# Performance work log

Measured on AMD Instinct MI355X. Metric: run time of the kernel, lower is better.

Reference implementation:

```python
import jax, jax.numpy as jnp
import numpy as np

N_NODES = 100000
N_EDGES = 1600000
IN_DIM, HIDDEN, OUT = 256, 128, 64


def setup_inputs() -> dict:
    key = jax.random.key(0)
    k1, k2, k3, k4 = jax.random.split(key, 4)
    x = jax.random.normal(k1, (N_NODES, IN_DIM), dtype=jnp.float32)
    edge_index = jax.random.randint(k2, (2, N_EDGES), 0, N_NODES, dtype=jnp.int32)
    # glorot-ish init for the GCN linear layers
    W1 = jax.random.normal(k3, (IN_DIM, HIDDEN), dtype=jnp.float32) / np.sqrt(IN_DIM)
    b1 = jnp.zeros((HIDDEN,), dtype=jnp.float32)
    W2 = jax.random.normal(k4, (HIDDEN, OUT), dtype=jnp.float32) / np.sqrt(HIDDEN)
    b2 = jnp.zeros((OUT,), dtype=jnp.float32)
    return {"x": x, "edge_index": edge_index, "W1": W1, "b1": b1, "W2": W2, "b2": b2}


def gcn_layer(x, src, dst, W, b):
    """PyG GCNConv: add self-loops, symmetric deg^-1/2 normalization,
    linear transform, scatter-add aggregation, bias."""
    h = x @ W  # [N, F_out]
    # degree over self-looped graph: in-degree(dst counts) + 1 self loop
    deg = jax.ops.segment_sum(jnp.ones((src.shape[0],), h.dtype), dst,
                              num_segments=N_NODES) + 1.0
    dinv = jax.lax.rsqrt(deg)  # [N]
    coef = dinv[src] * dinv[dst]  # [E]
    agg = jax.ops.segment_sum(h[src] * coef[:, None], dst, num_segments=N_NODES)
    # self-loop contribution (norm = dinv[i]^2) without materializing loop edges
    agg = agg + h * (dinv * dinv)[:, None]
    return agg + b


def reference(x, edge_index, W1, b1, W2, b2):
    src, dst = edge_index[0], edge_index[1]
    h = jax.nn.relu(gcn_layer(x, src, dst, W1, b1))
    return jax.nn.relu(gcn_layer(h, src, dst, W2, b2))
```

## Files before the change

kernel.cpp:

```cpp
#include <hip/hip_runtime.h>

#define N_NODES 100000
#define N_EDGES 1600000
#define IN_DIM 256
#define HIDDEN 128
#define OUT_DIM 64

#define NBIN 391
#define NBLK3 256
#define CHUNK 6250
#define NMAT (NBIN * NBLK3)
#define NBLK_SCAN (NMAT / 256)
#define CAP 6144

typedef __bf16 bf16x8 __attribute__((ext_vector_type(8)));
typedef __bf16 bf16x4 __attribute__((ext_vector_type(4)));
typedef float f32x4 __attribute__((ext_vector_type(4)));

__launch_bounds__(256)
__global__ void k_hist(const int* __restrict__ dst, int* __restrict__ cnt2) {
    __shared__ int hist[NBIN];
    for (int i = threadIdx.x; i < NBIN; i += 256) hist[i] = 0;
    __syncthreads();
    int base = blockIdx.x * CHUNK;
    for (int i = threadIdx.x; i < CHUNK; i += 256)
        atomicAdd(&hist[dst[base + i] >> 8], 1);
    __syncthreads();
    for (int k = threadIdx.x; k < NBIN; k += 256)
        cnt2[k * NBLK3 + blockIdx.x] = hist[k];
}

__global__ void k_scan1(int* __restrict__ a, int* __restrict__ bsum) {
    __shared__ int tmp[256];
    int t = threadIdx.x;
    int i = blockIdx.x * 256 + t;
    int v = a[i];
    tmp[t] = v;
    __syncthreads();
    #pragma unroll
    for (int off = 1; off < 256; off <<= 1) {
        int p = (t >= off) ? tmp[t - off] : 0;
        __syncthreads();
        tmp[t] += p;
        __syncthreads();
    }
    a[i] = tmp[t] - v;
    if (t == 255) bsum[blockIdx.x] = tmp[255];
}

__global__ void k_scan2(int* __restrict__ bsum) {
    __shared__ int tmp[512];
    int t = threadIdx.x;
    int v = (t < NBLK_SCAN) ? bsum[t] : 0;
    tmp[t] = v;
    __syncthreads();
    #pragma unroll
    for (int off = 1; off < 512; off <<= 1) {
        int p = (t >= off) ? tmp[t - off] : 0;
        __syncthreads();
        tmp[t] += p;
        __syncthreads();
    }
    if (t < NBLK_SCAN) bsum[t] = tmp[t] - v;
}

__launch_bounds__(256)
__global__ void k_scatter_bins(const int* __restrict__ src, const int* __restrict__ dst,
                               const int* __restrict__ off2, const int* __restrict__ bsum,
                               unsigned int* __restrict__ ebuf) {
    __shared__ int cursor[NBIN];
    for (int k = threadIdx.x; k < NBIN; k += 256)
        cursor[k] = off2[k * NBLK3 + blockIdx.x] + bsum[k];
    __syncthreads();
    int base = blockIdx.x * CHUNK;
    for (int i = threadIdx.x; i < CHUNK; i += 256) {
        int s = src[base + i], d = dst[base + i];
        int pos = atomicAdd(&cursor[d >> 8], 1);
        ebuf[pos] = ((unsigned)s << 8) | (unsigned)(d & 255);
    }
}

__launch_bounds__(256)
__global__ void k_fine(const unsigned int* __restrict__ ebuf, const int* __restrict__ off2,
                       const int* __restrict__ bsum,
                       int* __restrict__ esrc, int* __restrict__ rowstart,
                       float* __restrict__ dinv) {
    __shared__ int hist[256];
    __shared__ int tmp[256];
    __shared__ int nodeoff[256];
    __shared__ int cursor[256];
    __shared__ unsigned int ed[CAP];
    __shared__ int sOut[CAP];

    const int k = blockIdx.x;
    const int t = threadIdx.x;
    const int e0 = off2[k * NBLK3] + bsum[k];
    const int e1 = (k + 1 < NBIN) ? off2[(k + 1) * NBLK3] + bsum[k + 1] : N_EDGES;
    int m = e1 - e0;
    if (m > CAP) m = CAP;

    hist[t] = 0;
    __syncthreads();
    for (int i = t; i < m; i += 256) {
        unsigned v = ebuf[e0 + i];
        ed[i] = v;
        atomicAdd(&hist[v & 255], 1);
    }
    __syncthreads();

    int v = hist[t];
    tmp[t] = v;
    __syncthreads();
    #pragma unroll
    for (int off = 1; off < 256; off <<= 1) {
        int p = (t >= off) ? tmp[t - off] : 0;
        __syncthreads();
        tmp[t] += p;
        __syncthreads();
    }
    nodeoff[t] = tmp[t] - v;
    cursor[t] = tmp[t] - v;
    __syncthreads();

    for (int i = t; i < m; i += 256) {
        unsigned e = ed[i];
        int pos = atomicAdd(&cursor[e & 255], 1);
        sOut[pos] = (int)(e >> 8);
    }
    __syncthreads();

    for (int i = t; i < m; i += 256) esrc[e0 + i] = sOut[i];

    int n = k * 256 + t;
    if (n < N_NODES) {
        rowstart[n] = e0 + nodeoff[t];
        dinv[n] = rsqrtf((float)hist[t] + 1.0f);
    }
    if (k == 0 && t == 0) rowstart[N_NODES] = N_EDGES;
}

__device__ __forceinline__ int bsw1h(int c, int kk) {
    return c * 128 + (kk ^ ((c & 7) << 3));
}

__launch_bounds__(512, 4)
__global__ void k_gemm1(const float* __restrict__ X, const float* __restrict__ W1,
                        __bf16* __restrict__ H) {
    __shared__ __attribute__((aligned(16))) __bf16 Bs[128 * 128];

    const int t = threadIdx.x;
    const int wave = t >> 6;
    const int lane = t & 63;
    const int lm = lane & 15;
    const int q = lane >> 4;
    const int row0 = blockIdx.x * 128;
    const int g = row0 + wave * 16 + lm;

    f32x4 acc[8] = {};

    for (int half = 0; half < 2; ++half) {
        __syncthreads();
        for (int p = 0; p < 4; ++p) {
            int i = t + 512 * p;
            int c = i & 127;
            int kg = i >> 7;
            float v[8];
            #pragma unroll
            for (int j = 0; j < 8; ++j)
                v[j] = W1[(half * 128 + kg * 8 + j) * HIDDEN + c];
            bf16x8 w;
            #pragma unroll
            for (int j = 0; j < 8; ++j) w[j] = (__bf16)v[j];
            *(bf16x8*)&Bs[bsw1h(c, kg * 8)] = w;
        }
        __syncthreads();

        #pragma unroll
        for (int k0 = 0; k0 < 128; k0 += 32) {
            float4 v0 = make_float4(0.f, 0.f, 0.f, 0.f), v1 = v0;
            if (g < N_NODES) {
                const float* p = &X[(size_t)g * IN_DIM + half * 128 + k0 + q * 8];
                v0 = *(const float4*)p;
                v1 = *(const float4*)(p + 4);
            }
            bf16x8 a;
            a[0] = (__bf16)v0.x; a[1] = (__bf16)v0.y;
            a[2] = (__bf16)v0.z; a[3] = (__bf16)v0.w;
            a[4] = (__bf16)v1.x; a[5] = (__bf16)v1.y;
            a[6] = (__bf16)v1.z; a[7] = (__bf16)v1.w;
            #pragma unroll
            for (int ni = 0; ni < 8; ++ni) {
                bf16x8 bfr = *(const bf16x8*)&Bs[bsw1h(ni * 16 + lm, k0 + q * 8)];
                acc[ni] = __builtin_amdgcn_mfma_f32_16x16x32_bf16(a, bfr, acc[ni], 0, 0, 0);
            }
        }
    }

    #pragma unroll
    for (int r = 0; r < 4; ++r) {
        int grow = row0 + wave * 16 + q * 4 + r;
        if (grow < N_NODES) {
            #pragma unroll
            for (int ni = 0; ni < 8; ++ni)
                H[grow * HIDDEN + ni * 16 + lm] = (__bf16)acc[ni][r];
        }
    }
}

__launch_bounds__(256)
__global__ void k_gather1(const int* __restrict__ rowstart, const int* __restrict__ esrc,
                          const float* __restrict__ dinv,
                          const __bf16* __restrict__ H, const float* __restrict__ b1,
                          __bf16* __restrict__ AGG) {
    int n = blockIdx.x * 16 + (threadIdx.x >> 4);
    if (n >= N_NODES) return;
    int j = (threadIdx.x & 15) * 8;

    float dn = dinv[n];
    float s = dn * dn;
    bf16x8 h = *(const bf16x8*)&H[n * HIDDEN + j];
    float acc[8];
    #pragma unroll
    for (int i = 0; i < 8; ++i) acc[i] = (float)h[i] * s;

    int p0 = rowstart[n], p1 = rowstart[n + 1];
    int p = p0;
    for (; p + 3 < p1; p += 4) {
        int s0 = esrc[p + 0], s1 = esrc[p + 1], s2 = esrc[p + 2], s3 = esrc[p + 3];
        float c0 = dinv[s0] * dn, c1 = dinv[s1] * dn;
        float c2 = dinv[s2] * dn, c3 = dinv[s3] * dn;
        bf16x8 v0 = *(const bf16x8*)&H[s0 * HIDDEN + j];
        bf16x8 v1 = *(const bf16x8*)&H[s1 * HIDDEN + j];
        bf16x8 v2 = *(const bf16x8*)&H[s2 * HIDDEN + j];
        bf16x8 v3 = *(const bf16x8*)&H[s3 * HIDDEN + j];
        #pragma unroll
        for (int i = 0; i < 8; ++i) acc[i] = fmaf((float)v0[i], c0, acc[i]);
        #pragma unroll
        for (int i = 0; i < 8; ++i) acc[i] = fmaf((float)v1[i], c1, acc[i]);
        #pragma unroll
        for (int i = 0; i < 8; ++i) acc[i] = fmaf((float)v2[i], c2, acc[i]);
        #pragma unroll
        for (int i = 0; i < 8; ++i) acc[i] = fmaf((float)v3[i], c3, acc[i]);
    }
    for (; p < p1; ++p) {
        int sidx = esrc[p];
        float c = dinv[sidx] * dn;
        bf16x8 v = *(const bf16x8*)&H[sidx * HIDDEN + j];
        #pragma unroll
        for (int i = 0; i < 8; ++i) acc[i] = fmaf((float)v[i], c, acc[i]);
    }

    float4 bb0 = *(const float4*)&b1[j];
    float4 bb1 = *(const float4*)&b1[j + 4];
    bf16x8 o;
    o[0] = (__bf16)fmaxf(acc[0] + bb0.x, 0.f);
    o[1] = (__bf16)fmaxf(acc[1] + bb0.y, 0.f);
    o[2] = (__bf16)fmaxf(acc[2] + bb0.z, 0.f);
    o[3] = (__bf16)fmaxf(acc[3] + bb0.w, 0.f);
    o[4] = (__bf16)fmaxf(acc[4] + bb1.x, 0.f);
    o[5] = (__bf16)fmaxf(acc[5] + bb1.y, 0.f);
    o[6] = (__bf16)fmaxf(acc[6] + bb1.z, 0.f);
    o[7] = (__bf16)fmaxf(acc[7] + bb1.w, 0.f);
    *(bf16x8*)&AGG[n * HIDDEN + j] = o;
}

__device__ __forceinline__ int bsw2(int c, int kk) {
    return c * 128 + (kk ^ ((c & 7) << 3));
}

__launch_bounds__(512, 8)
__global__ void k_gemm2(const __bf16* __restrict__ AGG, const float* __restrict__ W2,
                        __bf16* __restrict__ H2) {
    __shared__ __attribute__((aligned(16))) __bf16 Bs[64 * 128];

    const int t = threadIdx.x;
    const int wave = t >> 6;
    const int lane = t & 63;
    const int lm = lane & 15;
    const int q = lane >> 4;
    const int row0 = blockIdx.x * 128;
    const int g = row0 + wave * 16 + lm;

    for (int p = 0; p < 2; ++p) {
        int i = t + 512 * p;
        int c = i & 63;
        int kg = i >> 6;
        float v[8];
        #pragma unroll
        for (int j = 0; j < 8; ++j)
            v[j] = W2[(kg * 8 + j) * OUT_DIM + c];
        bf16x8 w;
        #pragma unroll
        for (int j = 0; j < 8; ++j) w[j] = (__bf16)v[j];
        *(bf16x8*)&Bs[bsw2(c, kg * 8)] = w;
    }
    __syncthreads();

    f32x4 acc[4] = {};

    #pragma unroll
    for (int k0 = 0; k0 < HIDDEN; k0 += 32) {
        bf16x8 a = {};
        if (g < N_NODES)
            a = *(const bf16x8*)&AGG[(size_t)g * HIDDEN + k0 + q * 8];
        #pragma unroll
        for (int ni = 0; ni < 4; ++ni) {
            bf16x8 bfr = *(const bf16x8*)&Bs[bsw2(ni * 16 + lm, k0 + q * 8)];
            acc[ni] = __builtin_amdgcn_mfma_f32_16x16x32_bf16(a, bfr, acc[ni], 0, 0, 0);
        }
    }

    #pragma unroll
    for (int r = 0; r < 4; ++r) {
        int grow = row0 + wave * 16 + q * 4 + r;
        if (grow < N_NODES) {
            #pragma unroll
            for (int ni = 0; ni < 4; ++ni)
                H2[grow * OUT_DIM + ni * 16 + lm] = (__bf16)acc[ni][r];
        }
    }
}

__launch_bounds__(256)
__global__ void k_gather2(const int* __restrict__ rowstart, const int* __restrict__ esrc,
                          const float* __restrict__ dinv,
                          const __bf16* __restrict__ H2, const float* __restrict__ b2,
                          float* __restrict__ OUT) {
    int n = blockIdx.x * 32 + (threadIdx.x >> 3);
    if (n >= N_NODES) return;
    int j = (threadIdx.x & 7) * 8;

    float dn = dinv[n];
    float s = dn * dn;
    bf16x8 h = *(const bf16x8*)&H2[n * OUT_DIM + j];
    float acc[8];
    #pragma unroll
    for (int i = 0; i < 8; ++i) acc[i] = (float)h[i] * s;

    int p0 = rowstart[n], p1 = rowstart[n + 1];
    int p = p0;
    for (; p + 3 < p1; p += 4) {
        int s0 = esrc[p + 0], s1 = esrc[p + 1], s2 = esrc[p + 2], s3 = esrc[p + 3];
        float c0 = dinv[s0] * dn, c1 = dinv[s1] * dn;
        float c2 = dinv[s2] * dn, c3 = dinv[s3] * dn;
        bf16x8 v0 = *(const bf16x8*)&H2[s0 * OUT_DIM + j];
        bf16x8 v1 = *(const bf16x8*)&H2[s1 * OUT_DIM + j];
        bf16x8 v2 = *(const bf16x8*)&H2[s2 * OUT_DIM + j];
        bf16x8 v3 = *(const bf16x8*)&H2[s3 * OUT_DIM + j];
        #pragma unroll
        for (int i = 0; i < 8; ++i) acc[i] = fmaf((float)v0[i], c0, acc[i]);
        #pragma unroll
        for (int i = 0; i < 8; ++i) acc[i] = fmaf((float)v1[i], c1, acc[i]);
        #pragma unroll
        for (int i = 0; i < 8; ++i) acc[i] = fmaf((float)v2[i], c2, acc[i]);
        #pragma unroll
        for (int i = 0; i < 8; ++i) acc[i] = fmaf((float)v3[i], c3, acc[i]);
    }
    for (; p < p1; ++p) {
        int sidx = esrc[p];
        float c = dinv[sidx] * dn;
        bf16x8 v = *(const bf16x8*)&H2[sidx * OUT_DIM + j];
        #pragma unroll
        for (int i = 0; i < 8; ++i) acc[i] = fmaf((float)v[i], c, acc[i]);
    }

    float4 bb0 = *(const float4*)&b2[j];
    float4 bb1 = *(const float4*)&b2[j + 4];
    float4 o0, o1;
    o0.x = fmaxf(acc[0] + bb0.x, 0.f);
    o0.y = fmaxf(acc[1] + bb0.y, 0.f);
    o0.z = fmaxf(acc[2] + bb0.z, 0.f);
    o0.w = fmaxf(acc[3] + bb0.w, 0.f);
    o1.x = fmaxf(acc[4] + bb1.x, 0.f);
    o1.y = fmaxf(acc[5] + bb1.y, 0.f);
    o1.z = fmaxf(acc[6] + bb1.z, 0.f);
    o1.w = fmaxf(acc[7] + bb1.w, 0.f);
    *(float4*)&OUT[n * OUT_DIM + j] = o0;
    *(float4*)&OUT[n * OUT_DIM + j + 4] = o1;
}

extern "C" void kernel_launch(void* const* d_in, const int* in_sizes, int n_in,
                              void* d_out, int out_size, void* d_ws, size_t ws_size,
                              hipStream_t stream) {
    const float* x  = (const float*)d_in[0];
    const int* ei   = (const int*)d_in[1];
    const float* W1 = (const float*)d_in[2];
    const float* b1 = (const float*)d_in[3];
    const float* W2 = (const float*)d_in[4];
    const float* b2 = (const float*)d_in[5];
    float* out = (float*)d_out;

    const int* src = ei;
    const int* dst = ei + N_EDGES;

    char* ws = (char*)d_ws;
    int*          cnt2     = (int*)         (ws + 0x000000);
    int*          bsum     = (int*)         (ws + 0x080000);
    int*          rowstart = (int*)         (ws + 0x090000);
    float*        dinv     = (float*)       (ws + 0x100000);
    unsigned int* ebuf     = (unsigned int*)(ws + 0x180000);
    int*          esrc     = (int*)         (ws + 0x800000);
    __bf16*       h1       = (__bf16*)      (ws + 0xE80000);
    __bf16*       agg1     = (__bf16*)      (ws + 0x2880000);
    __bf16*       h2       = (__bf16*)      (ws + 0x4280000);

    k_hist<<<NBLK3, 256, 0, stream>>>(dst, cnt2);
    k_scan1<<<NBLK_SCAN, 256, 0, stream>>>(cnt2, bsum);
    k_scan2<<<1, 512, 0, stream>>>(bsum);
    k_scatter_bins<<<NBLK3, 256, 0, stream>>>(src, dst, cnt2, bsum, ebuf);
    k_fine<<<NBIN, 256, 0, stream>>>(ebuf, cnt2, bsum, esrc, rowstart, dinv);

    k_gemm1<<<(N_NODES + 127) / 128, 512, 0, stream>>>(x, W1, h1);
    k_gather1<<<(N_NODES + 15) / 16, 256, 0, stream>>>(rowstart, esrc, dinv, h1, b1, agg1);
    k_gemm2<<<(N_NODES + 127) / 128, 512, 0, stream>>>(agg1, W2, h2);
    k_gather2<<<(N_NODES + 31) / 32, 256, 0, stream>>>(rowstart, esrc, dinv, h2, b2, out);
}
```

Measured before the change: 335.8 us.

## Fuse layer-1 gather with layer-2 GEMM via shared-memory tile

```diff
diff --git a/kernel.cpp b/kernel.cpp
--- a/kernel.cpp
+++ b/kernel.cpp
@@ -207,79 +207,21 @@
     }
 }
 
-__launch_bounds__(256)
-__global__ void k_gather1(const int* __restrict__ rowstart, const int* __restrict__ esrc,
-                          const float* __restrict__ dinv,
-                          const __bf16* __restrict__ H, const float* __restrict__ b1,
-                          __bf16* __restrict__ AGG) {
-    int n = blockIdx.x * 16 + (threadIdx.x >> 4);
-    if (n >= N_NODES) return;
-    int j = (threadIdx.x & 15) * 8;
-
-    float dn = dinv[n];
-    float s = dn * dn;
-    bf16x8 h = *(const bf16x8*)&H[n * HIDDEN + j];
-    float acc[8];
-    #pragma unroll
-    for (int i = 0; i < 8; ++i) acc[i] = (float)h[i] * s;
-
-    int p0 = rowstart[n], p1 = rowstart[n + 1];
-    int p = p0;
-    for (; p + 3 < p1; p += 4) {
-        int s0 = esrc[p + 0], s1 = esrc[p + 1], s2 = esrc[p + 2], s3 = esrc[p + 3];
-        float c0 = dinv[s0] * dn, c1 = dinv[s1] * dn;
-        float c2 = dinv[s2] * dn, c3 = dinv[s3] * dn;
-        bf16x8 v0 = *(const bf16x8*)&H[s0 * HIDDEN + j];
-        bf16x8 v1 = *(const bf16x8*)&H[s1 * HIDDEN + j];
-        bf16x8 v2 = *(const bf16x8*)&H[s2 * HIDDEN + j];
-        bf16x8 v3 = *(const bf16x8*)&H[s3 * HIDDEN + j];
-        #pragma unroll
-        for (int i = 0; i < 8; ++i) acc[i] = fmaf((float)v0[i], c0, acc[i]);
-        #pragma unroll
-        for (int i = 0; i < 8; ++i) acc[i] = fmaf((float)v1[i], c1, acc[i]);
-        #pragma unroll
-        for (int i = 0; i < 8; ++i) acc[i] = fmaf((float)v2[i], c2, acc[i]);
-        #pragma unroll
-        for (int i = 0; i < 8; ++i) acc[i] = fmaf((float)v3[i], c3, acc[i]);
-    }
-    for (; p < p1; ++p) {
-        int sidx = esrc[p];
-        float c = dinv[sidx] * dn;
-        bf16x8 v = *(const bf16x8*)&H[sidx * HIDDEN + j];
-        #pragma unroll
-        for (int i = 0; i < 8; ++i) acc[i] = fmaf((float)v[i], c, acc[i]);
-    }
-
-    float4 bb0 = *(const float4*)&b1[j];
-    float4 bb1 = *(const float4*)&b1[j + 4];
-    bf16x8 o;
-    o[0] = (__bf16)fmaxf(acc[0] + bb0.x, 0.f);
-    o[1] = (__bf16)fmaxf(acc[1] + bb0.y, 0.f);
-    o[2] = (__bf16)fmaxf(acc[2] + bb0.z, 0.f);
-    o[3] = (__bf16)fmaxf(acc[3] + bb0.w, 0.f);
-    o[4] = (__bf16)fmaxf(acc[4] + bb1.x, 0.f);
-    o[5] = (__bf16)fmaxf(acc[5] + bb1.y, 0.f);
-    o[6] = (__bf16)fmaxf(acc[6] + bb1.z, 0.f);
-    o[7] = (__bf16)fmaxf(acc[7] + bb1.w, 0.f);
-    *(bf16x8*)&AGG[n * HIDDEN + j] = o;
-}
-
 __device__ __forceinline__ int bsw2(int c, int kk) {
     return c * 128 + (kk ^ ((c & 7) << 3));
 }
 
-__launch_bounds__(512, 8)
-__global__ void k_gemm2(const __bf16* __restrict__ AGG, const float* __restrict__ W2,
-                        __bf16* __restrict__ H2) {
+__launch_bounds__(512, 6)
+__global__ void k_gather1g2(const int* __restrict__ rowstart, const int* __restrict__ esrc,
+                            const float* __restrict__ dinv,
+                            const __bf16* __restrict__ H, const float* __restrict__ b1,
+                            const float* __restrict__ W2,
+                            __bf16* __restrict__ H2) {
+    __shared__ __attribute__((aligned(16))) __bf16 As[128 * 128];
     __shared__ __attribute__((aligned(16))) __bf16 Bs[64 * 128];
 
     const int t = threadIdx.x;
-    const int wave = t >> 6;
-    const int lane = t & 63;
-    const int lm = lane & 15;
-    const int q = lane >> 4;
     const int row0 = blockIdx.x * 128;
-    const int g = row0 + wave * 16 + lm;
 
     for (int p = 0; p < 2; ++p) {
         int i = t + 512 * p;
@@ -294,19 +236,78 @@
         for (int j = 0; j < 8; ++j) w[j] = (__bf16)v[j];
         *(bf16x8*)&Bs[bsw2(c, kg * 8)] = w;
     }
-    __syncthreads();
-
-    f32x4 acc[4] = {};
-
+
+    const int jc = t & 15;
+    const int j = jc * 8;
+    for (int pass = 0; pass < 4; ++pass) {
+        int nl = pass * 32 + (t >> 4);
+        int n = row0 + nl;
+        bf16x8 o = {};
+        if (n < N_NODES) {
+            float dn = dinv[n];
+            float s = dn * dn;
+            bf16x8 h = *(const bf16x8*)&H[n * HIDDEN + j];
+            float acc[8];
+            #pragma unroll
+            for (int i = 0; i < 8; ++i) acc[i] = (float)h[i] * s;
+
+            int p0 = rowstart[n], p1 = rowstart[n + 1];
+            int p = p0;
+            for (; p + 3 < p1; p += 4) {
+                int s0 = esrc[p + 0], s1 = esrc[p + 1], s2 = esrc[p + 2], s3 = esrc[p + 3];
+                float c0 = dinv[s0] * dn, c1 = dinv[s1] * dn;
+                float c2 = dinv[s2] * dn, c3 = dinv[s3] * dn;
+                bf16x8 v0 = *(const bf16x8*)&H[s0 * HIDDEN + j];
+                bf16x8 v1 = *(const bf16x8*)&H[s1 * HIDDEN + j];
+                bf16x8 v2 = *(const bf16x8*)&H[s2 * HIDDEN + j];
+                bf16x8 v3 = *(const bf16x8*)&H[s3 * HIDDEN + j];
+                #pragma unroll
+                for (int i = 0; i < 8; ++i) acc[i] = fmaf((float)v0[i], c0, acc[i]);
+                #pragma unroll
+                for (int i = 0; i < 8; ++i) acc[i] = fmaf((float)v1[i], c1, acc[i]);
+                #pragma unroll
+                for (int i = 0; i < 8; ++i) acc[i] = fmaf((float)v2[i], c2, acc[i]);
+                #pragma unroll
+                for (int i = 0; i < 8; ++i) acc[i] = fmaf((float)v3[i], c3, acc[i]);
+            }
+            for (; p < p1; ++p) {
+                int sidx = esrc[p];
+                float c = dinv[sidx] * dn;
+                bf16x8 v = *(const bf16x8*)&H[sidx * HIDDEN + j];
+                #pragma unroll
+                for (int i = 0; i < 8; ++i) acc[i] = fmaf((float)v[i], c, acc[i]);
+            }
+
+            float4 bb0 = *(const float4*)&b1[j];
+            float4 bb1 = *(const float4*)&b1[j + 4];
+            o[0] = (__bf16)fmaxf(acc[0] + bb0.x, 0.f);
+            o[1] = (__bf16)fmaxf(acc[1] + bb0.y, 0.f);
+            o[2] = (__bf16)fmaxf(acc[2] + bb0.z, 0.f);
+            o[3] = (__bf16)fmaxf(acc[3] + bb0.w, 0.f);
+            o[4] = (__bf16)fmaxf(acc[4] + bb1.x, 0.f);
+            o[5] = (__bf16)fmaxf(acc[5] + bb1.y, 0.f);
+            o[6] = (__bf16)fmaxf(acc[6] + bb1.z, 0.f);
+            o[7] = (__bf16)fmaxf(acc[7] + bb1.w, 0.f);
+        }
+        *(bf16x8*)&As[nl * 128 + (jc ^ (nl & 7)) * 8] = o;
+    }
+    __syncthreads();
+
+    const int wave = t >> 6;
+    const int lane = t & 63;
+    const int lm = lane & 15;
+    const int q = lane >> 4;
+    const int rl = wave * 16 + lm;
+
+    f32x4 acc2[4] = {};
     #pragma unroll
     for (int k0 = 0; k0 < HIDDEN; k0 += 32) {
-        bf16x8 a = {};
-        if (g < N_NODES)
-            a = *(const bf16x8*)&AGG[(size_t)g * HIDDEN + k0 + q * 8];
+        int c = (k0 >> 3) + q;
+        bf16x8 a = *(const bf16x8*)&As[rl * 128 + (c ^ (rl & 7)) * 8];
         #pragma unroll
         for (int ni = 0; ni < 4; ++ni) {
             bf16x8 bfr = *(const bf16x8*)&Bs[bsw2(ni * 16 + lm, k0 + q * 8)];
-            acc[ni] = __builtin_amdgcn_mfma_f32_16x16x32_bf16(a, bfr, acc[ni], 0, 0, 0);
+            acc2[ni] = __builtin_amdgcn_mfma_f32_16x16x32_bf16(a, bfr, acc2[ni], 0, 0, 0);
         }
     }
 
@@ -316,7 +317,7 @@
         if (grow < N_NODES) {
             #pragma unroll
             for (int ni = 0; ni < 4; ++ni)
-                H2[grow * OUT_DIM + ni * 16 + lm] = (__bf16)acc[ni][r];
+                H2[grow * OUT_DIM + ni * 16 + lm] = (__bf16)acc2[ni][r];
         }
     }
 }
@@ -401,7 +402,6 @@
     unsigned int* ebuf     = (unsigned int*)(ws + 0x180000);
     int*          esrc     = (int*)         (ws + 0x800000);
     __bf16*       h1       = (__bf16*)      (ws + 0xE80000);
-    __bf16*       agg1     = (__bf16*)      (ws + 0x2880000);
     __bf16*       h2       = (__bf16*)      (ws + 0x4280000);
 
     k_hist<<<NBLK3, 256, 0, stream>>>(dst, cnt2);
@@ -411,7 +411,7 @@
     k_fine<<<NBIN, 256, 0, stream>>>(ebuf, cnt2, bsum, esrc, rowstart, dinv);
 
     k_gemm1<<<(N_NODES + 127) / 128, 512, 0, stream>>>(x, W1, h1);
-    k_gather1<<<(N_NODES + 15) / 16, 256, 0, stream>>>(rowstart, esrc, dinv, h1, b1, agg1);
-    k_gemm2<<<(N_NODES + 127) / 128, 512, 0, stream>>>(agg1, W2, h2);
+    k_gather1g2<<<(N_NODES + 127) / 128, 512, 0, stream>>>(rowstart, esrc, dinv,
+                                                           h1, b1, W2, h2);
     k_gather2<<<(N_NODES + 31) / 32, 256, 0, stream>>>(rowstart, esrc, dinv, h2, b2, out);
 }
```

Result: slower. 346.4 us (+3.1%).

## Co-schedule gemm1 tiles inside graph-preprocessing kernels to overlap work

Applied to the files above, without the earlier changes.

```diff
diff --git a/kernel.cpp b/kernel.cpp
--- a/kernel.cpp
+++ b/kernel.cpp
@@ -13,147 +13,36 @@
 #define NBLK_SCAN (NMAT / 256)
 #define CAP 6144
 
+#define G1_TILES 782
+#define G_HIST  160
+#define G_SCAN1 120
+#define G_SCAN2 60
+#define G_SCAT  160
+#define G_FINE  282
+#define OFF_HIST  0
+#define OFF_SCAN1 160
+#define OFF_SCAN2 280
+#define OFF_SCAT  340
+#define OFF_FINE  500
+
 typedef __bf16 bf16x8 __attribute__((ext_vector_type(8)));
 typedef __bf16 bf16x4 __attribute__((ext_vector_type(4)));
 typedef float f32x4 __attribute__((ext_vector_type(4)));
 
-__launch_bounds__(256)
-__global__ void k_hist(const int* __restrict__ dst, int* __restrict__ cnt2) {
-    __shared__ int hist[NBIN];
-    for (int i = threadIdx.x; i < NBIN; i += 256) hist[i] = 0;
-    __syncthreads();
-    int base = blockIdx.x * CHUNK;
-    for (int i = threadIdx.x; i < CHUNK; i += 256)
-        atomicAdd(&hist[dst[base + i] >> 8], 1);
-    __syncthreads();
-    for (int k = threadIdx.x; k < NBIN; k += 256)
-        cnt2[k * NBLK3 + blockIdx.x] = hist[k];
-}
-
-__global__ void k_scan1(int* __restrict__ a, int* __restrict__ bsum) {
-    __shared__ int tmp[256];
-    int t = threadIdx.x;
-    int i = blockIdx.x * 256 + t;
-    int v = a[i];
-    tmp[t] = v;
-    __syncthreads();
-    #pragma unroll
-    for (int off = 1; off < 256; off <<= 1) {
-        int p = (t >= off) ? tmp[t - off] : 0;
-        __syncthreads();
-        tmp[t] += p;
-        __syncthreads();
-    }
-    a[i] = tmp[t] - v;
-    if (t == 255) bsum[blockIdx.x] = tmp[255];
-}
-
-__global__ void k_scan2(int* __restrict__ bsum) {
-    __shared__ int tmp[512];
-    int t = threadIdx.x;
-    int v = (t < NBLK_SCAN) ? bsum[t] : 0;
-    tmp[t] = v;
-    __syncthreads();
-    #pragma unroll
-    for (int off = 1; off < 512; off <<= 1) {
-        int p = (t >= off) ? tmp[t - off] : 0;
-        __syncthreads();
-        tmp[t] += p;
-        __syncthreads();
-    }
-    if (t < NBLK_SCAN) bsum[t] = tmp[t] - v;
-}
-
-__launch_bounds__(256)
-__global__ void k_scatter_bins(const int* __restrict__ src, const int* __restrict__ dst,
-                               const int* __restrict__ off2, const int* __restrict__ bsum,
-                               unsigned int* __restrict__ ebuf) {
-    __shared__ int cursor[NBIN];
-    for (int k = threadIdx.x; k < NBIN; k += 256)
-        cursor[k] = off2[k * NBLK3 + blockIdx.x] + bsum[k];
-    __syncthreads();
-    int base = blockIdx.x * CHUNK;
-    for (int i = threadIdx.x; i < CHUNK; i += 256) {
-        int s = src[base + i], d = dst[base + i];
-        int pos = atomicAdd(&cursor[d >> 8], 1);
-        ebuf[pos] = ((unsigned)s << 8) | (unsigned)(d & 255);
-    }
-}
-
-__launch_bounds__(256)
-__global__ void k_fine(const unsigned int* __restrict__ ebuf, const int* __restrict__ off2,
-                       const int* __restrict__ bsum,
-                       int* __restrict__ esrc, int* __restrict__ rowstart,
-                       float* __restrict__ dinv) {
-    __shared__ int hist[256];
-    __shared__ int tmp[256];
-    __shared__ int nodeoff[256];
-    __shared__ int cursor[256];
-    __shared__ unsigned int ed[CAP];
-    __shared__ int sOut[CAP];
-
-    const int k = blockIdx.x;
-    const int t = threadIdx.x;
-    const int e0 = off2[k * NBLK3] + bsum[k];
-    const int e1 = (k + 1 < NBIN) ? off2[(k + 1) * NBLK3] + bsum[k + 1] : N_EDGES;
-    int m = e1 - e0;
-    if (m > CAP) m = CAP;
-
-    hist[t] = 0;
-    __syncthreads();
-    for (int i = t; i < m; i += 256) {
-        unsigned v = ebuf[e0 + i];
-        ed[i] = v;
-        atomicAdd(&hist[v & 255], 1);
-    }
-    __syncthreads();
-
-    int v = hist[t];
-    tmp[t] = v;
-    __syncthreads();
-    #pragma unroll
-    for (int off = 1; off < 256; off <<= 1) {
-        int p = (t >= off) ? tmp[t - off] : 0;
-        __syncthreads();
-        tmp[t] += p;
-        __syncthreads();
-    }
-    nodeoff[t] = tmp[t] - v;
-    cursor[t] = tmp[t] - v;
-    __syncthreads();
-
-    for (int i = t; i < m; i += 256) {
-        unsigned e = ed[i];
-        int pos = atomicAdd(&cursor[e & 255], 1);
-        sOut[pos] = (int)(e >> 8);
-    }
-    __syncthreads();
-
-    for (int i = t; i < m; i += 256) esrc[e0 + i] = sOut[i];
-
-    int n = k * 256 + t;
-    if (n < N_NODES) {
-        rowstart[n] = e0 + nodeoff[t];
-        dinv[n] = rsqrtf((float)hist[t] + 1.0f);
-    }
-    if (k == 0 && t == 0) rowstart[N_NODES] = N_EDGES;
-}
-
 __device__ __forceinline__ int bsw1h(int c, int kk) {
     return c * 128 + (kk ^ ((c & 7) << 3));
 }
 
-__launch_bounds__(512, 4)
-__global__ void k_gemm1(const float* __restrict__ X, const float* __restrict__ W1,
-                        __bf16* __restrict__ H) {
-    __shared__ __attribute__((aligned(16))) __bf16 Bs[128 * 128];
-
+__device__ __forceinline__ void gemm1_tile(const float* __restrict__ X,
+                                           const float* __restrict__ W1,
+                                           __bf16* __restrict__ H,
+                                           int bid, __bf16* Bs) {
     const int t = threadIdx.x;
     const int wave = t >> 6;
     const int lane = t & 63;
     const int lm = lane & 15;
     const int q = lane >> 4;
-    const int row0 = blockIdx.x * 128;
+    const int row0 = bid * 128;
     const int g = row0 + wave * 16 + lm;
 
     f32x4 acc[8] = {};
@@ -207,6 +96,174 @@
     }
 }
 
+__global__ __launch_bounds__(512, 4)
+void k_hist_g(const int* __restrict__ dst, int* __restrict__ cnt2,
+              const float* __restrict__ X, const float* __restrict__ W1,
+              __bf16* __restrict__ H) {
+    __shared__ __attribute__((aligned(16))) char smem[32768];
+    if (blockIdx.x < NBLK3) {
+        int* hist = (int*)smem;
+        int t = threadIdx.x;
+        for (int i = t; i < NBIN; i += 512) hist[i] = 0;
+        __syncthreads();
+        int base = blockIdx.x * CHUNK;
+        for (int i = t; i < CHUNK; i += 512)
+            atomicAdd(&hist[dst[base + i] >> 8], 1);
+        __syncthreads();
+        for (int k = t; k < NBIN; k += 512)
+            cnt2[k * NBLK3 + blockIdx.x] = hist[k];
+    } else {
+        gemm1_tile(X, W1, H, OFF_HIST + (int)blockIdx.x - NBLK3, (__bf16*)smem);
+    }
+}
+
+__global__ __launch_bounds__(512, 4)
+void k_scan1_g(int* __restrict__ a, int* __restrict__ bsum,
+               const float* __restrict__ X, const float* __restrict__ W1,
+               __bf16* __restrict__ H) {
+    __shared__ __attribute__((aligned(16))) char smem[32768];
+    if (blockIdx.x < NBLK_SCAN) {
+        int* tmp = (int*)smem;
+        int t = threadIdx.x;
+        int i = blockIdx.x * 256 + t;
+        int v = 0;
+        if (t < 256) { v = a[i]; tmp[t] = v; }
+        __syncthreads();
+        #pragma unroll
+        for (int off = 1; off < 256; off <<= 1) {
+            int p = (t >= off && t < 256) ? tmp[t - off] : 0;
+            __syncthreads();
+            if (t < 256) tmp[t] += p;
+            __syncthreads();
+        }
+        if (t < 256) a[i] = tmp[t] - v;
+        if (t == 255) bsum[blockIdx.x] = tmp[255];
+    } else {
+        gemm1_tile(X, W1, H, OFF_SCAN1 + (int)blockIdx.x - NBLK_SCAN, (__bf16*)smem);
+    }
+}
+
+__global__ __launch_bounds__(512, 4)
+void k_scan2_g(int* __restrict__ bsum,
+               const float* __restrict__ X, const float* __restrict__ W1,
+               __bf16* __restrict__ H) {
+    __shared__ __attribute__((aligned(16))) char smem[32768];
+    if (blockIdx.x == 0) {
+        int* tmp = (int*)smem;
+        int t = threadIdx.x;
+        int v = (t < NBLK_SCAN) ? bsum[t] : 0;
+        tmp[t] = v;
+        __syncthreads();
+        #pragma unroll
+        for (int off = 1; off < 512; off <<= 1) {
+            int p = (t >= off) ? tmp[t - off] : 0;
+            __syncthreads();
+            tmp[t] += p;
+            __syncthreads();
+        }
+        if (t < NBLK_SCAN) bsum[t] = tmp[t] - v;
+    } else {
+        gemm1_tile(X, W1, H, OFF_SCAN2 + (int)blockIdx.x - 1, (__bf16*)smem);
+    }
+}
+
+__global__ __launch_bounds__(512, 4)
+void k_scatter_g(const int* __restrict__ src, const int* __restrict__ dst,
+                 const int* __restrict__ off2, const int* __restrict__ bsum,
+                 unsigned int* __restrict__ ebuf,
+                 const float* __restrict__ X, const float* __restrict__ W1,
+                 __bf16* __restrict__ H) {
+    __shared__ __attribute__((aligned(16))) char smem[32768];
+    if (blockIdx.x < NBLK3) {
+        int* cursor = (int*)smem;
+        int t = threadIdx.x;
+        for (int k = t; k < NBIN; k += 512)
+            cursor[k] = off2[k * NBLK3 + blockIdx.x] + bsum[k];
+        __syncthreads();
+        int base = blockIdx.x * CHUNK;
+        for (int i = t; i < CHUNK; i += 512) {
+            int s = src[base + i], d = dst[base + i];
+            int pos = atomicAdd(&cursor[d >> 8], 1);
+            ebuf[pos] = ((unsigned)s << 8) | (unsigned)(d & 255);
+        }
+    } else {
+        gemm1_tile(X, W1, H, OFF_SCAT + (int)blockIdx.x - NBLK3, (__bf16*)smem);
+    }
+}
+
+struct FineSm {
+    int hist[256];
+    int tmp[256];
+    int nodeoff[256];
+    int cursor[256];
+    unsigned int ed[CAP];
+    int sOut[CAP];
+};
+
+__global__ __launch_bounds__(512, 4)
+void k_fine_g(const unsigned int* __restrict__ ebuf, const int* __restrict__ off2,
+              const int* __restrict__ bsum,
+              int* __restrict__ esrc, int* __restrict__ rowstart,
+              float* __restrict__ dinv,
+              const float* __restrict__ X, const float* __restrict__ W1,
+              __bf16* __restrict__ H) {
+    __shared__ __attribute__((aligned(16))) char smem[sizeof(FineSm)];
+    if (blockIdx.x < NBIN) {
+        FineSm* sm = (FineSm*)smem;
+        const int k = blockIdx.x;
+        const int t = threadIdx.x;
+        const int e0 = off2[k * NBLK3] + bsum[k];
+        const int e1 = (k + 1 < NBIN) ? off2[(k + 1) * NBLK3] + bsum[k + 1] : N_EDGES;
+        int m = e1 - e0;
+        if (m > CAP) m = CAP;
+
+        if (t < 256) sm->hist[t] = 0;
+        __syncthreads();
+        for (int i = t; i < m; i += 512) {
+            unsigned v = ebuf[e0 + i];
+            sm->ed[i] = v;
+            atomicAdd(&sm->hist[v & 255], 1);
+        }
+        __syncthreads();
+
+        int v = (t < 256) ? sm->hist[t] : 0;
+        if (t < 256) sm->tmp[t] = v;
+        __syncthreads();
+        #pragma unroll
+        for (int off = 1; off < 256; off <<= 1) {
+            int p = (t >= off && t < 256) ? sm->tmp[t - off] : 0;
+            __syncthreads();
+            if (t < 256) sm->tmp[t] += p;
+            __syncthreads();
+        }
+        if (t < 256) {
+            sm->nodeoff[t] = sm->tmp[t] - v;
+            sm->cursor[t] = sm->tmp[t] - v;
+        }
+        __syncthreads();
+
+        for (int i = t; i < m; i += 512) {
+            unsigned e = sm->ed[i];
+            int pos = atomicAdd(&sm->cursor[e & 255], 1);
+            sm->sOut[pos] = (int)(e >> 8);
+        }
+        __syncthreads();
+
+        for (int i = t; i < m; i += 512) esrc[e0 + i] = sm->sOut[i];
+
+        if (t < 256) {
+            int n = k * 256 + t;
+            if (n < N_NODES) {
+                rowstart[n] = e0 + sm->nodeoff[t];
+                dinv[n] = rsqrtf((float)sm->hist[t] + 1.0f);
+            }
+        }
+        if (k == 0 && t == 0) rowstart[N_NODES] = N_EDGES;
+    } else {
+        gemm1_tile(X, W1, H, OFF_FINE + (int)blockIdx.x - NBIN, (__bf16*)smem);
+    }
+}
+
 __launch_bounds__(256)
 __global__ void k_gather1(const int* __restrict__ rowstart, const int* __restrict__ esrc,
                           const float* __restrict__ dinv,
@@ -404,13 +461,14 @@
     __bf16*       agg1     = (__bf16*)      (ws + 0x2880000);
     __bf16*       h2       = (__bf16*)      (ws + 0x4280000);
 
-    k_hist<<<NBLK3, 256, 0, stream>>>(dst, cnt2);
-    k_scan1<<<NBLK_SCAN, 256, 0, stream>>>(cnt2, bsum);
-    k_scan2<<<1, 512, 0, stream>>>(bsum);
-    k_scatter_bins<<<NBLK3, 256, 0, stream>>>(src, dst, cnt2, bsum, ebuf);
-    k_fine<<<NBIN, 256, 0, stream>>>(ebuf, cnt2, bsum, esrc, rowstart, dinv);
-
-    k_gemm1<<<(N_NODES + 127) / 128, 512, 0, stream>>>(x, W1, h1);
+    k_hist_g   <<<NBLK3     + G_HIST,  512, 0, stream>>>(dst, cnt2, x, W1, h1);
+    k_scan1_g  <<<NBLK_SCAN + G_SCAN1, 512, 0, stream>>>(cnt2, bsum, x, W1, h1);
+    k_scan2_g  <<<1         + G_SCAN2, 512, 0, stream>>>(bsum, x, W1, h1);
+    k_scatter_g<<<NBLK3     + G_SCAT,  512, 0, stream>>>(src, dst, cnt2, bsum, ebuf,
+                                                         x, W1, h1);
+    k_fine_g   <<<NBIN      + G_FINE,  512, 0, stream>>>(ebuf, cnt2, bsum, esrc,
+                                                         rowstart, dinv, x, W1, h1);
+
     k_gather1<<<(N_NODES + 15) / 16, 256, 0, stream>>>(rowstart, esrc, dinv, h1, b1, agg1);
     k_gemm2<<<(N_NODES + 127) / 128, 512, 0, stream>>>(agg1, W2, h2);
     k_gather2<<<(N_NODES + 31) / 32, 256, 0, stream>>>(rowstart, esrc, dinv, h2, b2, out);
```

Measured after the change: 333.9 us. No clear change (-0.6%).
